# Performance work log

Hardware: AMD Instinct MI355X
Metric: run time of the kernel (lower is better)

Reference implementation:

```python
import jax, jax.numpy as jnp
import numpy as np

NP_, NQ_, C_, E_ = 500000, 200000, 64, 1200000


def setup_inputs() -> dict:
    key = jax.random.key(0)
    ks = jax.random.split(key, 12)
    s = 0.1
    return {
        "x_person": jax.random.normal(ks[0], (NP_, C_), jnp.float32),
        "x_product": jax.random.normal(ks[1], (NQ_, C_), jnp.float32),
        "ei_pv_src": jax.random.randint(ks[2], (E_,), 0, NP_, jnp.int32),
        "ei_pv_dst": jax.random.randint(ks[3], (E_,), 0, NQ_, jnp.int32),
        "ei_vp_src": jax.random.randint(ks[4], (E_,), 0, NQ_, jnp.int32),
        "ei_vp_dst": jax.random.randint(ks[5], (E_,), 0, NP_, jnp.int32),
        "W_src": jax.random.normal(ks[6], (2, 2, C_, C_), jnp.float32) * s,
        "W_dst": jax.random.normal(ks[7], (2, 2, C_, C_), jnp.float32) * s,
        "a_src": jax.random.normal(ks[8], (2, 2, C_), jnp.float32) * s,
        "a_dst": jax.random.normal(ks[9], (2, 2, C_), jnp.float32) * s,
        "bias": jax.random.normal(ks[10], (2, 2, C_), jnp.float32) * s,
    }


def _gat_conv(x_src, x_dst, src, dst, Ws, Wd, avs, avd, b, n_dst):
    # PyG GATConv, heads=1, concat=False, add_self_loops=False, eval mode.
    hs = x_src @ Ws                       # [Ns, C]
    hd = x_dst @ Wd                       # [Nd, C]
    al_s = hs @ avs                       # [Ns]
    al_d = hd @ avd                       # [Nd]
    e = jax.nn.leaky_relu(al_s[src] + al_d[dst], 0.2)          # [E]
    m = jax.ops.segment_max(e, dst, num_segments=n_dst)        # segment softmax
    ex = jnp.exp(e - m[dst])
    den = jax.ops.segment_sum(ex, dst, num_segments=n_dst)
    alpha = ex / den[dst]                                      # [E]
    out = jax.ops.segment_sum(alpha[:, None] * hs[src], dst, num_segments=n_dst)
    return out + b


def reference(x_person, x_product, ei_pv_src, ei_pv_dst, ei_vp_src, ei_vp_dst,
              W_src, W_dst, a_src, a_dst, bias):
    hp, hq = x_person, x_product
    n_layers = W_src.shape[0]
    for l in range(n_layers):
        # edge type 0: Person -> Product (dst type Product)
        hq_new = _gat_conv(hp, hq, ei_pv_src, ei_pv_dst,
                           W_src[l, 0], W_dst[l, 0], a_src[l, 0], a_dst[l, 0],
                           bias[l, 0], NQ_)
        # edge type 1: Product -> Person (dst type Person)
        hp_new = _gat_conv(hq, hp, ei_vp_src, ei_vp_dst,
                           W_src[l, 1], W_dst[l, 1], a_src[l, 1], a_dst[l, 1],
                           bias[l, 1], NP_)
        hp, hq = hp_new, hq_new
        if l < n_layers - 1:
            hp = jax.nn.elu(hp)  # dropout is identity in eval mode
            hq = jax.nn.elu(hq)
    # final_projection is Identity (gat_heads == 1), then ELU
    return jax.nn.elu(hp), jax.nn.elu(hq)
```

## Files before the change

kernel.cpp:

```cpp
#include <hip/hip_runtime.h>
#include <hip/hip_bf16.h>
#include <math.h>

#define NP 500000
#define NQ 200000
#define C 64
#define NE 1200000
#define TILE 64
#define PADC 66


__global__ void wdavd_kernel(const float* __restrict__ Wd,
                             const float* __restrict__ avd,
                             float* __restrict__ wv) {
    int k = threadIdx.x;
    if (k < C) {
        float acc = 0.f;
        #pragma unroll
        for (int j = 0; j < C; ++j) acc = fmaf(Wd[k * C + j], avd[j], acc);
        wv[k] = acc;
    }
}

__global__ void __launch_bounds__(256) hs_kernel(
        const float* __restrict__ x, const float* __restrict__ W,
        const float* __restrict__ avs,
        __hip_bfloat16* __restrict__ hs, float* __restrict__ al_s, int Ns) {
    __shared__ float xt_all[4][TILE * PADC];
    const int widb = threadIdx.x >> 6;
    const int lane = threadIdx.x & 63;
    float* xt = xt_all[widb];
    const int gwave  = blockIdx.x * 4 + widb;
    const int nwaves = gridDim.x * 4;
    const int ntiles = (Ns + TILE - 1) / TILE;

    for (int tile = gwave; tile < ntiles; tile += nwaves) {
        const int row0  = tile * TILE;
        const int valid = Ns - row0;
        const bool full = (valid >= TILE);
        const float* xb = x + (size_t)row0 * C;

        #pragma unroll 8
        for (int i = 0; i < 32; ++i) {
            int e = i * 128 + lane * 2;
            int r = e >> 6, c0 = e & 63;
            float2 v = make_float2(0.f, 0.f);
            if (full || r < valid) v = *(const float2*)(xb + e);
            *(float2*)(xt + r * PADC + c0) = v;
        }
        asm volatile("s_waitcnt lgkmcnt(0)" ::: "memory");

        float acc[C];
        #pragma unroll
        for (int c = 0; c < C; ++c) acc[c] = 0.f;
        const float* xrow = xt + lane * PADC;

        for (int kk = 0; kk < 32; ++kk) {
            float2 xv = *(const float2*)(xrow + 2 * kk);
            #pragma unroll
            for (int c = 0; c < C; ++c)
                acc[c] = fmaf(xv.x, W[(2 * kk) * C + c], acc[c]);
            #pragma unroll
            for (int c = 0; c < C; ++c)
                acc[c] = fmaf(xv.y, W[(2 * kk + 1) * C + c], acc[c]);
        }

        if (full || lane < valid) {
            float s = 0.f;
            #pragma unroll
            for (int c = 0; c < C; ++c) s = fmaf(acc[c], avs[c], s);
            al_s[row0 + lane] = s;

            uint32_t pk[32];
            #pragma unroll
            for (int j = 0; j < 32; ++j) {
                __hip_bfloat16 lo = __float2bfloat16(acc[2 * j]);
                __hip_bfloat16 hi = __float2bfloat16(acc[2 * j + 1]);
                pk[j] = (uint32_t)(*(uint16_t*)&lo) | ((uint32_t)(*(uint16_t*)&hi) << 16);
            }
            uint32_t* hrow = (uint32_t*)(hs + (size_t)(row0 + lane) * C);
            #pragma unroll
            for (int j = 0; j < 8; ++j)
                *(uint4*)(hrow + 4 * j) = *(const uint4*)(pk + 4 * j);
        }
    }
}

__global__ void __launch_bounds__(256) ald_kernel(
        const float* __restrict__ x, const float* __restrict__ wv,
        float* __restrict__ al_d, int Nd) {
    const int lane = threadIdx.x & 63;
    const int sub  = lane & 15;
    const int wid  = (blockIdx.x * 256 + threadIdx.x) >> 6;
    const int nw   = gridDim.x * 4;
    const float4 w4 = *(const float4*)(wv + sub * 4);
    const int nquad = (Nd + 3) >> 2;
    for (int q = wid; q < nquad; q += nw) {
        int row = q * 4 + (lane >> 4);
        float s = 0.f;
        if (row < Nd) {
            float4 v4 = *(const float4*)(x + (size_t)row * C + sub * 4);
            s = v4.x * w4.x + v4.y * w4.y + v4.z * w4.z + v4.w * w4.w;
        }
        s += __shfl_xor(s, 1); s += __shfl_xor(s, 2);
        s += __shfl_xor(s, 4); s += __shfl_xor(s, 8);
        if (sub == 0 && row < Nd) al_d[row] = s;
    }
}

__global__ void __launch_bounds__(256) edge1_kernel(
        const int* __restrict__ src, const int* __restrict__ dst,
        const float* __restrict__ al_s, const float* __restrict__ al_d,
        float* __restrict__ exb, float* __restrict__ den) {
    int e = blockIdx.x * 256 + threadIdx.x;
    if (e >= NE) return;
    int s = src[e], d = dst[e];
    float v = al_s[s] + al_d[d];
    v = v > 0.f ? v : 0.2f * v;
    float xv = expf(v);
    exb[e] = xv;
    atomicAdd(&den[d], xv);
}

__global__ void __launch_bounds__(256) edge2_kernel(
        const int* __restrict__ src, const int* __restrict__ dst,
        const float* __restrict__ exb, const float* __restrict__ den,
        const __hip_bfloat16* __restrict__ hs, float* __restrict__ agg) {
    int lane = threadIdx.x & 63;
    int e = (blockIdx.x * 256 + threadIdx.x) >> 6;
    if (e >= NE) return;
    int s = src[e], d = dst[e];
    float alpha = exb[e] / den[d];
    float v = alpha * __bfloat162float(hs[(size_t)s * C + lane]);
    atomicAdd(&agg[(size_t)d * C + lane], v);
}

__global__ void __launch_bounds__(256) finish_f32_kernel(
        float* __restrict__ agg, const float* __restrict__ bias, int n) {
    int i = blockIdx.x * 256 + threadIdx.x;
    int stride = gridDim.x * 256;
    for (; i < n; i += stride) {
        float v = agg[i] + bias[i & (C - 1)];
        agg[i] = v > 0.f ? v : expm1f(v);
    }
}


static inline int imin(int a, int b) { return a < b ? a : b; }

extern "C" void kernel_launch(void* const* d_in, const int* in_sizes, int n_in,
                              void* d_out, int out_size, void* d_ws, size_t ws_size,
                              hipStream_t stream) {
    const float* x_person  = (const float*)d_in[0];
    const float* x_product = (const float*)d_in[1];
    const int* pv_src = (const int*)d_in[2];
    const int* pv_dst = (const int*)d_in[3];
    const int* vp_src = (const int*)d_in[4];
    const int* vp_dst = (const int*)d_in[5];
    const float* W_src = (const float*)d_in[6];
    const float* W_dst = (const float*)d_in[7];
    const float* a_src = (const float*)d_in[8];
    const float* a_dst = (const float*)d_in[9];
    const float* bias  = (const float*)d_in[10];

    float* hp1 = (float*)d_ws;
    float* hq1 = hp1 + (size_t)NP * C;
    __hip_bfloat16* hs = (__hip_bfloat16*)(hq1 + (size_t)NQ * C);
    float* den  = (float*)(hs + (size_t)NP * C);
    float* al_s = den + NP;
    float* al_d = al_s + NP;
    float* exb  = al_d + NP;
    float* wv   = exb + NE;

    float* out_hp = (float*)d_out;
    float* out_hq = out_hp + (size_t)NP * C;

    auto run_conv = [&](const float* xsrc, int Ns, const float* xdst, int Nd,
                        const int* esrc, const int* edst,
                        int l, int et, float* aggbuf) {
        const float* Ws  = W_src + (size_t)(l * 2 + et) * C * C;
        const float* Wd  = W_dst + (size_t)(l * 2 + et) * C * C;
        const float* avs = a_src + (size_t)(l * 2 + et) * C;
        const float* avd = a_dst + (size_t)(l * 2 + et) * C;

        hipMemsetAsync(den, 0, (size_t)Nd * sizeof(float), stream);
        hipMemsetAsync(aggbuf, 0, (size_t)Nd * C * sizeof(float), stream);

        int ntiles = (Ns + TILE - 1) / TILE;
        wdavd_kernel<<<1, 64, 0, stream>>>(Wd, avd, wv);
        hs_kernel<<<imin((ntiles + 3) / 4, 4096), 256, 0, stream>>>(xsrc, Ws, avs, hs, al_s, Ns);
        ald_kernel<<<imin((((Nd + 3) / 4) + 3) / 4, 2048), 256, 0, stream>>>(xdst, wv, al_d, Nd);
        edge1_kernel<<<(NE + 255) / 256, 256, 0, stream>>>(esrc, edst, al_s, al_d, exb, den);
        edge2_kernel<<<NE / 4, 256, 0, stream>>>(esrc, edst, exb, den, hs, aggbuf);
    };

    run_conv(x_person, NP, x_product, NQ, pv_src, pv_dst, 0, 0, hq1);
    finish_f32_kernel<<<2048, 256, 0, stream>>>(hq1, bias + 0 * C, NQ * C);
    run_conv(x_product, NQ, x_person, NP, vp_src, vp_dst, 0, 1, hp1);
    finish_f32_kernel<<<2048, 256, 0, stream>>>(hp1, bias + 1 * C, NP * C);

    run_conv(hp1, NP, hq1, NQ, pv_src, pv_dst, 1, 0, out_hq);
    finish_f32_kernel<<<2048, 256, 0, stream>>>(out_hq, bias + 2 * C, NQ * C);
    run_conv(hq1, NQ, hp1, NP, vp_src, vp_dst, 1, 1, out_hp);
    finish_f32_kernel<<<2048, 256, 0, stream>>>(out_hp, bias + 3 * C, NP * C);
}
```

Baseline: 2.423 ms.

## Build CSR by destination once and fuse softmax, aggregation and ELU per node

The change builds a destination-sorted CSR for both edge types once per call, using a histogram, a wave-level scan with an atomic base allocation, and an atomic scatter. A per-destination wavefront kernel then computes the softmax denominator and the weighted gather of hs, and applies bias plus ELU in registers. This replaces the per-edge atomicAdd into den and the 64-wide atomic scatter into agg, and it also drops the memsets, the exb buffer and the separate finish passes. In exchange it adds a CSR build cost, recomputes exp in two passes over neighbours, and gives uneven work per wave when node degrees vary.

```diff
diff --git a/kernel.cpp b/kernel.cpp
--- a/kernel.cpp
+++ b/kernel.cpp
@@ -8,6 +8,42 @@
 #define NE 1200000
 #define TILE 64
 #define PADC 66
+
+
+__global__ void __launch_bounds__(256) hist_kernel(
+        const int* __restrict__ dst, int* __restrict__ cnt) {
+    int e = blockIdx.x * 256 + threadIdx.x;
+    if (e < NE) atomicAdd(&cnt[dst[e]], 1);
+}
+
+__global__ void __launch_bounds__(256) alloc_kernel(
+        int* __restrict__ cnt, int* __restrict__ start,
+        int* __restrict__ gcur, int n) {
+    int i = blockIdx.x * 256 + threadIdx.x;
+    int lane = threadIdx.x & 63;
+    int c = (i < n) ? cnt[i] : 0;
+    int sc = c;
+    #pragma unroll
+    for (int off = 1; off < 64; off <<= 1) {
+        int t = __shfl_up(sc, off);
+        if (lane >= off) sc += t;
+    }
+    int total = __shfl(sc, 63);
+    int base = 0;
+    if (lane == 63) base = atomicAdd(gcur, total);
+    base = __shfl(base, 63);
+    int st = base + sc - c;
+    if (i < n) { start[i] = st; cnt[i] = st; }
+}
+
+__global__ void __launch_bounds__(256) scatter_kernel(
+        const int* __restrict__ src, const int* __restrict__ dst,
+        int* __restrict__ cur, int* __restrict__ srcv) {
+    int e = blockIdx.x * 256 + threadIdx.x;
+    if (e >= NE) return;
+    int pos = atomicAdd(&cur[dst[e]], 1);
+    srcv[pos] = src[e];
+}
 
 
 __global__ void wdavd_kernel(const float* __restrict__ Wd,
@@ -108,40 +144,36 @@
     }
 }
 
-__global__ void __launch_bounds__(256) edge1_kernel(
-        const int* __restrict__ src, const int* __restrict__ dst,
+__global__ void __launch_bounds__(256) gat_csr_kernel(
+        const int* __restrict__ start, const int* __restrict__ endp,
+        const int* __restrict__ srcv,
         const float* __restrict__ al_s, const float* __restrict__ al_d,
-        float* __restrict__ exb, float* __restrict__ den) {
-    int e = blockIdx.x * 256 + threadIdx.x;
-    if (e >= NE) return;
-    int s = src[e], d = dst[e];
-    float v = al_s[s] + al_d[d];
-    v = v > 0.f ? v : 0.2f * v;
-    float xv = expf(v);
-    exb[e] = xv;
-    atomicAdd(&den[d], xv);
-}
-
-__global__ void __launch_bounds__(256) edge2_kernel(
-        const int* __restrict__ src, const int* __restrict__ dst,
-        const float* __restrict__ exb, const float* __restrict__ den,
-        const __hip_bfloat16* __restrict__ hs, float* __restrict__ agg) {
-    int lane = threadIdx.x & 63;
-    int e = (blockIdx.x * 256 + threadIdx.x) >> 6;
-    if (e >= NE) return;
-    int s = src[e], d = dst[e];
-    float alpha = exb[e] / den[d];
-    float v = alpha * __bfloat162float(hs[(size_t)s * C + lane]);
-    atomicAdd(&agg[(size_t)d * C + lane], v);
-}
-
-__global__ void __launch_bounds__(256) finish_f32_kernel(
-        float* __restrict__ agg, const float* __restrict__ bias, int n) {
-    int i = blockIdx.x * 256 + threadIdx.x;
-    int stride = gridDim.x * 256;
-    for (; i < n; i += stride) {
-        float v = agg[i] + bias[i & (C - 1)];
-        agg[i] = v > 0.f ? v : expm1f(v);
+        const __hip_bfloat16* __restrict__ hs, const float* __restrict__ bias,
+        float* __restrict__ out, int Nd) {
+    const int lane = threadIdx.x & 63;
+    const int wid  = (blockIdx.x * 256 + threadIdx.x) >> 6;
+    const int nw   = gridDim.x * 4;
+    const float b  = bias[lane];
+    for (int d = wid; d < Nd; d += nw) {
+        const int st = start[d], en = endp[d];
+        const float ad = al_d[d];
+        float den = 0.f;
+        for (int j = st; j < en; ++j) {
+            float v = al_s[srcv[j]] + ad;
+            v = v > 0.f ? v : 0.2f * v;
+            den += expf(v);
+        }
+        const float rden = (en > st) ? 1.f / den : 0.f;
+        float acc = 0.f;
+        for (int j = st; j < en; ++j) {
+            int s = srcv[j];
+            float v = al_s[s] + ad;
+            v = v > 0.f ? v : 0.2f * v;
+            float w = expf(v) * rden;
+            acc = fmaf(w, __bfloat162float(hs[(size_t)s * C + lane]), acc);
+        }
+        float o = acc + b;
+        out[(size_t)d * C + lane] = o > 0.f ? o : expm1f(o);
     }
 }
 
@@ -163,44 +195,53 @@
     const float* a_dst = (const float*)d_in[9];
     const float* bias  = (const float*)d_in[10];
 
-    float* hp1 = (float*)d_ws;
-    float* hq1 = hp1 + (size_t)NP * C;
-    __hip_bfloat16* hs = (__hip_bfloat16*)(hq1 + (size_t)NQ * C);
-    float* den  = (float*)(hs + (size_t)NP * C);
-    float* al_s = den + NP;
-    float* al_d = al_s + NP;
-    float* exb  = al_d + NP;
-    float* wv   = exb + NE;
-
     float* out_hp = (float*)d_out;
     float* out_hq = out_hp + (size_t)NP * C;
 
+    float* hp1 = out_hp;
+    float* hq1 = (float*)d_ws;
+    __hip_bfloat16* hs = (__hip_bfloat16*)(hq1 + (size_t)NQ * C);
+    float* al_s = (float*)(hs + (size_t)NP * C);
+    float* al_d = al_s + NP;
+    float* wv   = al_d + NP;
+    int* gcur   = (int*)(wv + C);
+    int* start_pv = gcur + 2;
+    int* cur_pv   = start_pv + NQ;
+    int* srcv_pv  = cur_pv + NQ;
+    int* start_vp = srcv_pv + NE;
+    int* cur_vp   = start_vp + NP;
+    int* srcv_vp  = cur_vp + NP;
+
+    hipMemsetAsync(cur_pv, 0, (size_t)NQ * sizeof(int), stream);
+    hipMemsetAsync(cur_vp, 0, (size_t)NP * sizeof(int), stream);
+    hipMemsetAsync(gcur, 0, 2 * sizeof(int), stream);
+    hist_kernel<<<(NE + 255) / 256, 256, 0, stream>>>(pv_dst, cur_pv);
+    hist_kernel<<<(NE + 255) / 256, 256, 0, stream>>>(vp_dst, cur_vp);
+    alloc_kernel<<<(NQ + 255) / 256, 256, 0, stream>>>(cur_pv, start_pv, gcur + 0, NQ);
+    alloc_kernel<<<(NP + 255) / 256, 256, 0, stream>>>(cur_vp, start_vp, gcur + 1, NP);
+    scatter_kernel<<<(NE + 255) / 256, 256, 0, stream>>>(pv_src, pv_dst, cur_pv, srcv_pv);
+    scatter_kernel<<<(NE + 255) / 256, 256, 0, stream>>>(vp_src, vp_dst, cur_vp, srcv_vp);
+
     auto run_conv = [&](const float* xsrc, int Ns, const float* xdst, int Nd,
-                        const int* esrc, const int* edst,
-                        int l, int et, float* aggbuf) {
+                        const int* startA, const int* endA, const int* srcvA,
+                        int l, int et, float* outbuf) {
         const float* Ws  = W_src + (size_t)(l * 2 + et) * C * C;
         const float* Wd  = W_dst + (size_t)(l * 2 + et) * C * C;
         const float* avs = a_src + (size_t)(l * 2 + et) * C;
         const float* avd = a_dst + (size_t)(l * 2 + et) * C;
-
-        hipMemsetAsync(den, 0, (size_t)Nd * sizeof(float), stream);
-        hipMemsetAsync(aggbuf, 0, (size_t)Nd * C * sizeof(float), stream);
+        const float* bia = bias  + (size_t)(l * 2 + et) * C;
 
         int ntiles = (Ns + TILE - 1) / TILE;
         wdavd_kernel<<<1, 64, 0, stream>>>(Wd, avd, wv);
         hs_kernel<<<imin((ntiles + 3) / 4, 4096), 256, 0, stream>>>(xsrc, Ws, avs, hs, al_s, Ns);
         ald_kernel<<<imin((((Nd + 3) / 4) + 3) / 4, 2048), 256, 0, stream>>>(xdst, wv, al_d, Nd);
-        edge1_kernel<<<(NE + 255) / 256, 256, 0, stream>>>(esrc, edst, al_s, al_d, exb, den);
-        edge2_kernel<<<NE / 4, 256, 0, stream>>>(esrc, edst, exb, den, hs, aggbuf);
+        gat_csr_kernel<<<imin((Nd + 3) / 4, 16384), 256, 0, stream>>>(
+            startA, endA, srcvA, al_s, al_d, hs, bia, outbuf, Nd);
     };
 
-    run_conv(x_person, NP, x_product, NQ, pv_src, pv_dst, 0, 0, hq1);
-    finish_f32_kernel<<<2048, 256, 0, stream>>>(hq1, bias + 0 * C, NQ * C);
-    run_conv(x_product, NQ, x_person, NP, vp_src, vp_dst, 0, 1, hp1);
-    finish_f32_kernel<<<2048, 256, 0, stream>>>(hp1, bias + 1 * C, NP * C);
-
-    run_conv(hp1, NP, hq1, NQ, pv_src, pv_dst, 1, 0, out_hq);
-    finish_f32_kernel<<<2048, 256, 0, stream>>>(out_hq, bias + 2 * C, NQ * C);
-    run_conv(hq1, NQ, hp1, NP, vp_src, vp_dst, 1, 1, out_hp);
-    finish_f32_kernel<<<2048, 256, 0, stream>>>(out_hp, bias + 3 * C, NP * C);
-}
+    run_conv(x_person, NP, x_product, NQ, start_pv, cur_pv, srcv_pv, 0, 0, hq1);
+    run_conv(x_product, NQ, x_person, NP, start_vp, cur_vp, srcv_vp, 0, 1, hp1);
+
+    run_conv(hp1, NP, hq1, NQ, start_pv, cur_pv, srcv_pv, 1, 0, out_hq);
+    run_conv(hq1, NQ, hp1, NP, start_vp, cur_vp, srcv_vp, 1, 1, out_hp);
+}
```

Measured after the change: 2.199 ms. 9.3% less time.
